# Kernel tuning notes

Hardware: AMD Instinct MI355X
Metric: run time of the kernel (lower is better)

The kernel has to match this reference:

```python
import jax, jax.numpy as jnp
import numpy as np

SCALE = 1.0

def _sq_dist(p0, p1):
    # p0: [B,N,3], p1: [B,M,3] -> [B,N,M] squared euclidean distances
    n0 = jnp.sum(p0 * p0, axis=-1)  # [B,N]
    n1 = jnp.sum(p1 * p1, axis=-1)  # [B,M]
    inner = jnp.einsum('bnd,bmd->bnm', p0, p1)  # [B,N,M]
    return n0[:, :, None] + n1[:, None, :] - 2.0 * inner

def setup_inputs() -> dict:
    key = jax.random.key(0)
    k0, k1 = jax.random.split(key)
    template = jax.random.normal(k0, (4, 8192, 3), dtype=jnp.float32)
    source = jax.random.normal(k1, (4, 8192, 3), dtype=jnp.float32)
    return {"template": template, "source": source}

def reference(template, source):
    p0 = template / SCALE
    p1 = source / SCALE
    d = _sq_dist(p0, p1)  # [B,N,M]
    # nearest neighbor in each direction, averaged over points
    d01 = jnp.mean(jnp.min(d, axis=2), axis=1)  # template -> source, [B]
    d10 = jnp.mean(jnp.min(d, axis=1), axis=1)  # source -> template, [B]
    return d01 + d10  # per-batch chamfer distance (reduction='none')
```

## Files before the change

### kernel.cpp

```cpp
#include <hip/hip_runtime.h>
#include <stdint.h>


typedef __bf16 bf16x8 __attribute__((ext_vector_type(8)));
typedef float  f32x16 __attribute__((ext_vector_type(16)));

constexpr int B     = 4;
constexpr int NPTS  = 8192;
constexpr int BLOCK = 256;
constexpr int QPW   = 64;
constexpr int QPB   = 256;
constexpr int QBLKS = NPTS / QPB;
constexpr int CH    = 4;
constexpr int CPTS  = NPTS / CH;
constexpr int SPTS  = 512;
constexpr int NPASS = CPTS / SPTS;
constexpr int TPP   = SPTS / 32;
constexpr int PASSBYTES = SPTS * 2 * 16;
constexpr size_t KEYBYTES = (size_t)2 * B * NPTS * sizeof(unsigned);

__device__ inline unsigned key_of(float f) {
    unsigned b = __float_as_uint(f);
    return b ^ (unsigned)(((int)b >> 31) | (int)0x80000000u);
}
__device__ inline float float_of(unsigned k) {
    unsigned b = (k & 0x80000000u) ? (k ^ 0x80000000u) : ~k;
    return __uint_as_float(b);
}

__device__ inline void gload_lds16(const void* g, void* l) {
    __builtin_amdgcn_global_load_lds(
        (const __attribute__((address_space(1))) uint32_t*)g,
        (__attribute__((address_space(3))) uint32_t*)l, 16, 0, 0);
}

__global__ __launch_bounds__(BLOCK) void chamfer_prep(
    const float* __restrict__ tpl, const float* __restrict__ src,
    bf16x8* __restrict__ efrag,
    unsigned* __restrict__ keys, float* __restrict__ out)
{
    const int pt  = blockIdx.x * BLOCK + threadIdx.x;
    const int c   = blockIdx.y;
    const int b   = c & (B - 1);
    const int dir = c >> 2;
    const float* db = (dir == 0 ? src : tpl) + (size_t)b * NPTS * 3;

    keys[(size_t)c * NPTS + pt] = 0u;
    if (blockIdx.x == 0 && c == 0 && threadIdx.x < B) out[threadIdx.x] = 0.f;

    float x = db[3 * pt], y = db[3 * pt + 1], z = db[3 * pt + 2];
    float n = -0.5f * (x * x + y * y + z * z);
    __bf16 hx = (__bf16)x, hy = (__bf16)y, hz = (__bf16)z;
    __bf16 lx = (__bf16)(x - (float)hx);
    __bf16 ly = (__bf16)(y - (float)hy);
    __bf16 lz = (__bf16)(z - (float)hz);
    __bf16 nh = (__bf16)n;
    __bf16 nl = (__bf16)(n - (float)nh);
    const __bf16 zb = (__bf16)0.0f;

    size_t base = ((size_t)c * NPTS + pt) * 2;
    efrag[base]     = (bf16x8){hx, hy, hz, lx, ly, lz, hx, hy};
    efrag[base + 1] = (bf16x8){hz, nh, nl, lx, ly, lz, zb, zb};
}

__global__ __launch_bounds__(BLOCK, 4) void chamfer_sweep(
    const float* __restrict__ tpl, const float* __restrict__ src,
    const bf16x8* __restrict__ efrag,
    unsigned* __restrict__ keys)
{
    __shared__ bf16x8 sbuf[2][SPTS * 2];

    const int tid = threadIdx.x;
    const int l   = tid & 63;
    const int w   = tid >> 6;
    const int h   = l >> 5;
    const int r32 = l & 31;
    const int c   = blockIdx.z;
    const int b   = c & (B - 1);
    const int dir = c >> 2;
    const float* q = (dir == 0 ? tpl : src) + (size_t)b * NPTS * 3;
    const int qbase = blockIdx.x * QPB + w * QPW;
    const char* eb  = (const char*)(efrag + ((size_t)c * NPTS + blockIdx.y * CPTS) * 2);

    #pragma unroll
    for (int i = 0; i < 4; ++i) {
        int off = (w * 4 + i) * 1024;
        gload_lds16(eb + off + l * 16, (char*)&sbuf[0][0] + off);
    }

    const __bf16 one = (__bf16)1.0f, zb = (__bf16)0.0f;
    bf16x8 fa[2];
    #pragma unroll
    for (int f = 0; f < 2; ++f) {
        int qi = qbase + f * 32 + r32;
        float x = q[3 * qi], y = q[3 * qi + 1], z = q[3 * qi + 2];
        __bf16 hx = (__bf16)x, hy = (__bf16)y, hz = (__bf16)z;
        __bf16 lx = (__bf16)(x - (float)hx);
        __bf16 ly = (__bf16)(y - (float)hy);
        __bf16 lz = (__bf16)(z - (float)hz);
        if (h == 0) fa[f] = (bf16x8){hx, hy, hz, hx, hy, hz, lx, ly};
        else        fa[f] = (bf16x8){lz, one, one, lx, ly, lz, zb, zb};
    }

    f32x16 best0, best1, zc;
    #pragma unroll
    for (int r = 0; r < 16; ++r) { best0[r] = -3.4e38f; best1[r] = -3.4e38f; zc[r] = 0.0f; }

    const int idx = r32 * 2 + h;
    for (int p = 0; p < NPASS; ++p) {
        __syncthreads();
        if (p + 1 < NPASS) {
            const char* ebn = eb + (p + 1) * PASSBYTES;
            char* dst = (char*)&sbuf[(p + 1) & 1][0];
            #pragma unroll
            for (int i = 0; i < 4; ++i) {
                int off = (w * 4 + i) * 1024;
                gload_lds16(ebn + off + l * 16, dst + off);
            }
        }
        const bf16x8* sb = sbuf[p & 1];
        #pragma unroll
        for (int t = 0; t < TPP; t += 2) {
            bf16x8 bv0 = sb[t * 64 + idx];
            bf16x8 bv1 = sb[(t + 1) * 64 + idx];
            f32x16 d00 = __builtin_amdgcn_mfma_f32_32x32x16_bf16(fa[0], bv0, zc, 0, 0, 0);
            f32x16 d01 = __builtin_amdgcn_mfma_f32_32x32x16_bf16(fa[0], bv1, zc, 0, 0, 0);
            #pragma unroll
            for (int r = 0; r < 16; ++r)
                best0[r] = fmaxf(fmaxf(best0[r], d00[r]), d01[r]);
            f32x16 d10 = __builtin_amdgcn_mfma_f32_32x32x16_bf16(fa[1], bv0, zc, 0, 0, 0);
            f32x16 d11 = __builtin_amdgcn_mfma_f32_32x32x16_bf16(fa[1], bv1, zc, 0, 0, 0);
            #pragma unroll
            for (int r = 0; r < 16; ++r)
                best1[r] = fmaxf(fmaxf(best1[r], d10[r]), d11[r]);
        }
    }

    #pragma unroll
    for (int m = 1; m < 32; m <<= 1) {
        #pragma unroll
        for (int r = 0; r < 16; ++r) {
            best0[r] = fmaxf(best0[r], __shfl_xor(best0[r], m, 64));
            best1[r] = fmaxf(best1[r], __shfl_xor(best1[r], m, 64));
        }
    }
    if (r32 == 0) {
        unsigned* kz = keys + (size_t)c * NPTS;
        #pragma unroll
        for (int r = 0; r < 16; ++r) {
            int row = (r & 3) + 8 * (r >> 2) + 4 * h;
            atomicMax(&kz[qbase + row],      key_of(best0[r]));
            atomicMax(&kz[qbase + 32 + row], key_of(best1[r]));
        }
    }
}

__global__ __launch_bounds__(256) void chamfer_final(
    const float* __restrict__ tpl, const float* __restrict__ src,
    const unsigned* __restrict__ keys, float* __restrict__ out)
{
    __shared__ float red[256];
    const int z = blockIdx.x;
    const float* qc = (z < B ? tpl : src) + (size_t)(z & (B - 1)) * NPTS * 3;

    float s = 0.f;
    for (int i = threadIdx.x; i < NPTS; i += 256) {
        float md = float_of(keys[(size_t)z * NPTS + i]);
        float x = qc[3 * i], y = qc[3 * i + 1], zz = qc[3 * i + 2];
        s += fmaf(md, -2.0f, x * x + y * y + zz * zz);
    }
    red[threadIdx.x] = s;
    __syncthreads();
    #pragma unroll
    for (int off = 128; off > 0; off >>= 1) {
        if (threadIdx.x < off) red[threadIdx.x] += red[threadIdx.x + off];
        __syncthreads();
    }
    if (threadIdx.x == 0)
        atomicAdd(&out[z & (B - 1)], red[0] * (1.0f / NPTS));
}

extern "C" void kernel_launch(void* const* d_in, const int* in_sizes, int n_in,
                              void* d_out, int out_size, void* d_ws, size_t ws_size,
                              hipStream_t stream) {
    const float* tpl = (const float*)d_in[0];
    const float* src = (const float*)d_in[1];
    float* out = (float*)d_out;
    unsigned* keys = (unsigned*)d_ws;
    bf16x8* efrag  = (bf16x8*)((char*)d_ws + KEYBYTES);

    chamfer_prep <<<dim3(NPTS / BLOCK, 2 * B), BLOCK, 0, stream>>>(tpl, src, efrag, keys, out);
    chamfer_sweep<<<dim3(QBLKS, CH, 2 * B),    BLOCK, 0, stream>>>(tpl, src, efrag, keys);
    chamfer_final<<<2 * B, 256, 0, stream>>>(tpl, src, keys, out);
}
```

Measured before the change: 43.98 us.

## Replace shuffle-and-atomicMax epilogue with LDS transpose reduction and per-chunk partial maxima

The sweep epilogue stops doing a five-step cross-lane shuffle reduction followed by atomicMax on order-preserving integer keys. It now writes the MFMA accumulators to padded LDS, has each thread reduce one query row, and stores per-chunk maxima to a workspace that the final kernel combines. The prep layout is regrouped so each 32-point group keeps its two fragment halves contiguous, giving conflict-free LDS B-operand reads. sched_barriers are added to pin MFMA and max interleaving. This removes the keys zero-init and atomics at the cost of a larger workspace and four reads per point in the final kernel.

```diff
diff --git a/kernel.cpp b/kernel.cpp
--- a/kernel.cpp
+++ b/kernel.cpp
@@ -4,6 +4,7 @@
 
 typedef __bf16 bf16x8 __attribute__((ext_vector_type(8)));
 typedef float  f32x16 __attribute__((ext_vector_type(16)));
+typedef float  f32x4  __attribute__((ext_vector_type(4)));
 
 constexpr int B     = 4;
 constexpr int NPTS  = 8192;
@@ -16,17 +17,10 @@
 constexpr int SPTS  = 512;
 constexpr int NPASS = CPTS / SPTS;
 constexpr int TPP   = SPTS / 32;
-constexpr int PASSBYTES = SPTS * 2 * 16;
-constexpr size_t KEYBYTES = (size_t)2 * B * NPTS * sizeof(unsigned);
-
-__device__ inline unsigned key_of(float f) {
-    unsigned b = __float_as_uint(f);
-    return b ^ (unsigned)(((int)b >> 31) | (int)0x80000000u);
-}
-__device__ inline float float_of(unsigned k) {
-    unsigned b = (k & 0x80000000u) ? (k ^ 0x80000000u) : ~k;
-    return __uint_as_float(b);
-}
+constexpr int GRPS  = NPTS / 32;
+constexpr int RSTRIDE = 36;
+constexpr int SMEMB = BLOCK * RSTRIDE * 4;
+constexpr size_t CMBYTES = (size_t)2 * B * CH * NPTS * sizeof(float);
 
 __device__ inline void gload_lds16(const void* g, void* l) {
     __builtin_amdgcn_global_load_lds(
@@ -36,8 +30,7 @@
 
 __global__ __launch_bounds__(BLOCK) void chamfer_prep(
     const float* __restrict__ tpl, const float* __restrict__ src,
-    bf16x8* __restrict__ efrag,
-    unsigned* __restrict__ keys, float* __restrict__ out)
+    bf16x8* __restrict__ efrag, float* __restrict__ out)
 {
     const int pt  = blockIdx.x * BLOCK + threadIdx.x;
     const int c   = blockIdx.y;
@@ -45,7 +38,6 @@
     const int dir = c >> 2;
     const float* db = (dir == 0 ? src : tpl) + (size_t)b * NPTS * 3;
 
-    keys[(size_t)c * NPTS + pt] = 0u;
     if (blockIdx.x == 0 && c == 0 && threadIdx.x < B) out[threadIdx.x] = 0.f;
 
     float x = db[3 * pt], y = db[3 * pt + 1], z = db[3 * pt + 2];
@@ -58,17 +50,18 @@
     __bf16 nl = (__bf16)(n - (float)nh);
     const __bf16 zb = (__bf16)0.0f;
 
-    size_t base = ((size_t)c * NPTS + pt) * 2;
-    efrag[base]     = (bf16x8){hx, hy, hz, lx, ly, lz, hx, hy};
-    efrag[base + 1] = (bf16x8){hz, nh, nl, lx, ly, lz, zb, zb};
+    const int gi = pt >> 5, sl = pt & 31;
+    size_t gb = ((size_t)c * GRPS + gi) * 64;
+    efrag[gb + sl]      = (bf16x8){hx, hy, hz, lx, ly, lz, hx, hy};
+    efrag[gb + 32 + sl] = (bf16x8){hz, nh, nl, lx, ly, lz, zb, zb};
 }
 
 __global__ __launch_bounds__(BLOCK, 4) void chamfer_sweep(
     const float* __restrict__ tpl, const float* __restrict__ src,
     const bf16x8* __restrict__ efrag,
-    unsigned* __restrict__ keys)
+    float* __restrict__ cm)
 {
-    __shared__ bf16x8 sbuf[2][SPTS * 2];
+    __shared__ char smem[SMEMB];
 
     const int tid = threadIdx.x;
     const int l   = tid & 63;
@@ -80,12 +73,13 @@
     const int dir = c >> 2;
     const float* q = (dir == 0 ? tpl : src) + (size_t)b * NPTS * 3;
     const int qbase = blockIdx.x * QPB + w * QPW;
-    const char* eb  = (const char*)(efrag + ((size_t)c * NPTS + blockIdx.y * CPTS) * 2);
+    const char* eb  = (const char*)efrag
+                    + ((size_t)c * GRPS + blockIdx.y * (CPTS / 32)) * 1024;
 
     #pragma unroll
     for (int i = 0; i < 4; ++i) {
         int off = (w * 4 + i) * 1024;
-        gload_lds16(eb + off + l * 16, (char*)&sbuf[0][0] + off);
+        gload_lds16(eb + off + l * 16, smem + off);
     }
 
     const __bf16 one = (__bf16)1.0f, zb = (__bf16)0.0f;
@@ -106,66 +100,70 @@
     #pragma unroll
     for (int r = 0; r < 16; ++r) { best0[r] = -3.4e38f; best1[r] = -3.4e38f; zc[r] = 0.0f; }
 
-    const int idx = r32 * 2 + h;
+    const int idx0 = h * 32 + r32;
     for (int p = 0; p < NPASS; ++p) {
         __syncthreads();
         if (p + 1 < NPASS) {
-            const char* ebn = eb + (p + 1) * PASSBYTES;
-            char* dst = (char*)&sbuf[(p + 1) & 1][0];
+            const char* ebn = eb + (size_t)(p + 1) * SPTS * 2 * 16;
+            char* dst = smem + ((p + 1) & 1) * 16384;
             #pragma unroll
             for (int i = 0; i < 4; ++i) {
                 int off = (w * 4 + i) * 1024;
                 gload_lds16(ebn + off + l * 16, dst + off);
             }
         }
-        const bf16x8* sb = sbuf[p & 1];
+        const bf16x8* sb = (const bf16x8*)(smem + (p & 1) * 16384);
         #pragma unroll
         for (int t = 0; t < TPP; t += 2) {
-            bf16x8 bv0 = sb[t * 64 + idx];
-            bf16x8 bv1 = sb[(t + 1) * 64 + idx];
-            f32x16 d00 = __builtin_amdgcn_mfma_f32_32x32x16_bf16(fa[0], bv0, zc, 0, 0, 0);
-            f32x16 d01 = __builtin_amdgcn_mfma_f32_32x32x16_bf16(fa[0], bv1, zc, 0, 0, 0);
+            bf16x8 bv0 = sb[t * 64 + idx0];
+            bf16x8 bv1 = sb[(t + 1) * 64 + idx0];
+            f32x16 d0 = __builtin_amdgcn_mfma_f32_32x32x16_bf16(fa[0], bv0, zc, 0, 0, 0);
+            f32x16 d1 = __builtin_amdgcn_mfma_f32_32x32x16_bf16(fa[0], bv1, zc, 0, 0, 0);
             #pragma unroll
             for (int r = 0; r < 16; ++r)
-                best0[r] = fmaxf(fmaxf(best0[r], d00[r]), d01[r]);
-            f32x16 d10 = __builtin_amdgcn_mfma_f32_32x32x16_bf16(fa[1], bv0, zc, 0, 0, 0);
-            f32x16 d11 = __builtin_amdgcn_mfma_f32_32x32x16_bf16(fa[1], bv1, zc, 0, 0, 0);
+                best0[r] = fmaxf(fmaxf(best0[r], d0[r]), d1[r]);
+            __builtin_amdgcn_sched_barrier(0);
+            d0 = __builtin_amdgcn_mfma_f32_32x32x16_bf16(fa[1], bv0, zc, 0, 0, 0);
+            d1 = __builtin_amdgcn_mfma_f32_32x32x16_bf16(fa[1], bv1, zc, 0, 0, 0);
             #pragma unroll
             for (int r = 0; r < 16; ++r)
-                best1[r] = fmaxf(fmaxf(best1[r], d10[r]), d11[r]);
+                best1[r] = fmaxf(fmaxf(best1[r], d1[r]), d0[r]);
+            __builtin_amdgcn_sched_barrier(0);
         }
     }
 
+    __syncthreads();
+    float* red = (float*)smem;
     #pragma unroll
-    for (int m = 1; m < 32; m <<= 1) {
-        #pragma unroll
-        for (int r = 0; r < 16; ++r) {
-            best0[r] = fmaxf(best0[r], __shfl_xor(best0[r], m, 64));
-            best1[r] = fmaxf(best1[r], __shfl_xor(best1[r], m, 64));
-        }
+    for (int r = 0; r < 16; ++r) {
+        int row = (r & 3) + 8 * (r >> 2) + 4 * h;
+        red[(w * 64 + row) * RSTRIDE + r32]      = best0[r];
+        red[(w * 64 + 32 + row) * RSTRIDE + r32] = best1[r];
     }
-    if (r32 == 0) {
-        unsigned* kz = keys + (size_t)c * NPTS;
-        #pragma unroll
-        for (int r = 0; r < 16; ++r) {
-            int row = (r & 3) + 8 * (r >> 2) + 4 * h;
-            atomicMax(&kz[qbase + row],      key_of(best0[r]));
-            atomicMax(&kz[qbase + 32 + row], key_of(best1[r]));
-        }
+    __syncthreads();
+    const float* rr = red + tid * RSTRIDE;
+    float m = -3.4e38f;
+    #pragma unroll
+    for (int j = 0; j < 8; ++j) {
+        f32x4 v = *(const f32x4*)(rr + 4 * j);
+        m = fmaxf(m, fmaxf(fmaxf(v.x, v.y), fmaxf(v.z, v.w)));
     }
+    cm[((size_t)c * CH + blockIdx.y) * NPTS + blockIdx.x * QPB + tid] = m;
 }
 
 __global__ __launch_bounds__(256) void chamfer_final(
     const float* __restrict__ tpl, const float* __restrict__ src,
-    const unsigned* __restrict__ keys, float* __restrict__ out)
+    const float* __restrict__ cm, float* __restrict__ out)
 {
     __shared__ float red[256];
     const int z = blockIdx.x;
     const float* qc = (z < B ? tpl : src) + (size_t)(z & (B - 1)) * NPTS * 3;
+    const float* cz = cm + (size_t)z * CH * NPTS;
 
     float s = 0.f;
     for (int i = threadIdx.x; i < NPTS; i += 256) {
-        float md = float_of(keys[(size_t)z * NPTS + i]);
+        float md = fmaxf(fmaxf(cz[i], cz[NPTS + i]),
+                         fmaxf(cz[2 * NPTS + i], cz[3 * NPTS + i]));
         float x = qc[3 * i], y = qc[3 * i + 1], zz = qc[3 * i + 2];
         s += fmaf(md, -2.0f, x * x + y * y + zz * zz);
     }
@@ -186,10 +184,10 @@
     const float* tpl = (const float*)d_in[0];
     const float* src = (const float*)d_in[1];
     float* out = (float*)d_out;
-    unsigned* keys = (unsigned*)d_ws;
-    bf16x8* efrag  = (bf16x8*)((char*)d_ws + KEYBYTES);
+    float* cm      = (float*)d_ws;
+    bf16x8* efrag  = (bf16x8*)((char*)d_ws + CMBYTES);
 
-    chamfer_prep <<<dim3(NPTS / BLOCK, 2 * B), BLOCK, 0, stream>>>(tpl, src, efrag, keys, out);
-    chamfer_sweep<<<dim3(QBLKS, CH, 2 * B),    BLOCK, 0, stream>>>(tpl, src, efrag, keys);
-    chamfer_final<<<2 * B, 256, 0, stream>>>(tpl, src, keys, out);
+    chamfer_prep <<<dim3(NPTS / BLOCK, 2 * B), BLOCK, 0, stream>>>(tpl, src, efrag, out);
+    chamfer_sweep<<<dim3(QBLKS, CH, 2 * B),    BLOCK, 0, stream>>>(tpl, src, efrag, cm);
+    chamfer_final<<<2 * B, 256, 0, stream>>>(tpl, src, cm, out);
 }
```

Result: faster. 39.78 us (-9.5%).
